# Performance work log

Hardware: AMD Instinct MI355X
Metric: run time of the kernel (lower is better)

The kernel has to match this reference:

```python
import jax, jax.numpy as jnp
import numpy as np

H, W = 512, 512
N = H * W
NCLS = 4
D_BI, D_SP = 5, 2
THETA_ALPHA, THETA_BETA, THETA_GAMMA = 80.0, 0.0625, 3.0
BI_COMPAT, SP_COMPAT, COMPATIBILITY = 10.0, 3.0, -1.0
NUM_ITER = 10


def _build_lattice(feats):
    """Permutohedral lattice precompute (numpy, integer index construction).
    feats: [N, d]. Returns os [N,d+1] int32 (1-based), ws [N,d+1] float32,
    bn [d+1, M, 2] int32 (0 = missing neighbor), M."""
    feats = np.asarray(feats, np.float64)
    n, d = feats.shape
    inv_std = np.sqrt(2.0 / 3.0) * (d + 1)
    scale = inv_std / np.sqrt((np.arange(d) + 1.0) * (np.arange(d) + 2.0))
    cf = feats * scale
    # embedding matrix E: elevated = cf @ E.T lies on the hyperplane sum=0
    E = np.zeros((d + 1, d))
    E[0, :] = 1.0
    for j in range(1, d + 1):
        E[j, j:] = 1.0
        E[j, j - 1] = -j
    elevated = cf @ E.T  # [n, d+1]
    greedy = (np.rint(elevated / (d + 1)) * (d + 1)).astype(np.int64)
    diff = elevated - greedy
    idx = np.arange(d + 1)
    upper = idx[None, :] > idx[:, None]
    lower = idx[None, :] < idx[:, None]
    di = diff[:, :, None]
    dj = diff[:, None, :]
    rank = (((dj > di) & upper) | ((dj >= di) & lower)).sum(-1)
    rank = rank + greedy.sum(1, keepdims=True) // (d + 1)
    low = rank < 0
    rank = rank + np.where(low, d + 1, 0)
    greedy = greedy + np.where(low, d + 1, 0)
    high = rank > d
    rank = rank - np.where(high, d + 1, 0)
    greedy = greedy - np.where(high, d + 1, 0)
    # barycentric weights
    bary = np.zeros((n, d + 2))
    v = (elevated - greedy) / (d + 1)
    rows = np.repeat(np.arange(n), d + 1)
    np.add.at(bary, (rows, (d - rank).ravel()), v.ravel())
    np.add.at(bary, (rows, (d + 1 - rank).ravel()), -v.ravel())
    bary[:, 0] += 1.0 + bary[:, d + 1]
    ws = bary[:, : d + 1].astype(np.float32)
    # simplex vertex keys (first d coords; last is implied by zero-sum)
    keys = np.empty((n, d + 1, d), np.int64)
    for r in range(d + 1):
        keys[:, r, :] = (greedy + r - (d + 1) * (rank > d - r))[:, :d]
    flat = keys.reshape(-1, d)
    lo = flat.min(0) - (d + 1)
    hi = flat.max(0) + (d + 1)
    strides = np.cumprod(np.concatenate([[1], (hi - lo + 1)[:-1]]))
    coords = (flat - lo) @ strides
    uniq, first, inv = np.unique(coords, return_index=True, return_inverse=True)
    M = int(len(uniq))
    os_ = (inv.reshape(n, d + 1) + 1).astype(np.int32)
    ukeys = flat[first]
    bn = np.zeros((d + 1, M, 2), np.int32)
    for j in range(d + 1):
        n1 = ukeys - 1
        n2 = ukeys + 1
        if j < d:
            n1[:, j] = ukeys[:, j] + d
            n2[:, j] = ukeys[:, j] - d
        for t, nk in enumerate((n1, n2)):
            c = (nk - lo) @ strides
            pos = np.clip(np.searchsorted(uniq, c), 0, M - 1)
            bn[j, :, t] = np.where(uniq[pos] == c, pos + 1, 0)
    return os_, ws, bn, M


def setup_inputs() -> dict:
    key = jax.random.key(0)
    k1, k2 = jax.random.split(key)
    image = jax.random.uniform(k1, (H, W, 7), dtype=jnp.float32)
    unary = jax.random.normal(k2, (H, W, NCLS), dtype=jnp.float32)
    img = np.asarray(image)
    yy, xx = np.mgrid[0:H, 0:W].astype(np.float64)
    bifeat = np.concatenate(
        [(xx / THETA_ALPHA)[..., None], (yy / THETA_ALPHA)[..., None],
         img[..., :3] / THETA_BETA], axis=-1).reshape(N, D_BI)
    spfeat = np.stack([xx / THETA_GAMMA, yy / THETA_GAMMA], -1).reshape(N, D_SP)
    os_b, ws_b, bn_b, M_b = _build_lattice(bifeat)
    os_s, ws_s, bn_s, M_s = _build_lattice(spfeat)
    return {
        "unary": unary,
        "ws_bilateral": jnp.asarray(ws_b), "os_bilateral": jnp.asarray(os_b),
        "blur_neighbors_bilateral": jnp.asarray(bn_b), "M_bilateral": M_b,
        "ws_spatial": jnp.asarray(ws_s), "os_spatial": jnp.asarray(os_s),
        "blur_neighbors_spatial": jnp.asarray(bn_s), "M_spatial": M_s,
    }


def _perm_filter(values, os_, ws, bn, M, alpha):
    # values: [N, C]; splat -> blur -> slice
    d1 = os_.shape[1]
    C = values.shape[1]
    table = jnp.zeros((M + 1, C), values.dtype)  # row 0 = dummy (missing)
    table = table.at[os_.reshape(-1)].add(
        (values[:, None, :] * ws[:, :, None]).reshape(-1, C))
    for j in range(d1):  # [0.5, 1, 0.5] blur along each lattice axis
        table = table.at[1:].add(0.5 * (table[bn[j, :, 0]] + table[bn[j, :, 1]]))
    return alpha * jnp.einsum("nrc,nr->nc", table[os_], ws)


def _mean_field(unary, ws_b, os_b, bn_b, M_b, ws_s, os_s, bn_s, M_s):
    C = unary.shape[-1]
    u = unary.reshape(N, C)
    alpha_b = 1.0 / (1.0 + 2.0 ** (-D_BI))
    alpha_s = 1.0 / (1.0 + 2.0 ** (-D_SP))
    ones = jnp.ones((N, 1), u.dtype)
    inv_nb = 1.0 / (_perm_filter(ones, os_b, ws_b, bn_b, M_b, alpha_b) + 1e-20)
    inv_ns = 1.0 / (_perm_filter(ones, os_s, ws_s, bn_s, M_s, alpha_s) + 1e-20)
    Q = jax.nn.softmax(-u, axis=-1)
    for _ in range(NUM_ITER):
        msg = (BI_COMPAT * _perm_filter(Q, os_b, ws_b, bn_b, M_b, alpha_b) * inv_nb
               + SP_COMPAT * _perm_filter(Q, os_s, ws_s, bn_s, M_s, alpha_s) * inv_ns)
        Q = jax.nn.softmax(-u - COMPATIBILITY * msg, axis=-1)
    return Q.reshape(H, W, C)


def reference(unary, ws_bilateral, os_bilateral, blur_neighbors_bilateral, M_bilateral,
              ws_spatial, os_spatial, blur_neighbors_spatial, M_spatial):
    # Returns the refined marginals Q [H, W, NCLS]; the module's MAP output is
    # jnp.argmax(Q, -1) (kept soft here so fwd/bwd share one output).
    return _mean_field(unary, ws_bilateral, os_bilateral, blur_neighbors_bilateral,
                       M_bilateral, ws_spatial, os_spatial, blur_neighbors_spatial,
                       M_spatial)
```

## Files before the change

kernel.cpp:

```cpp
#include <hip/hip_runtime.h>

#define NPIX (512 * 512)
#define BLK 256

#define SCAN_T 256
#define SCAN_E 8
#define SCAN_CHUNK (SCAN_T * SCAN_E)

constexpr float ALPHA_B = 32.0f / 33.0f;
constexpr float ALPHA_S = 0.8f;
constexpr float BI_COMPAT = 10.0f;
constexpr float SP_COMPAT = 3.0f;

__device__ __forceinline__ unsigned pack_ent(int n, float w) {
    float wc = fminf(fmaxf(w, 0.f), 1.f);
    unsigned iw = (unsigned)(wc * 16383.f + 0.5f);
    return (iw << 18) | (unsigned)n;
}
__device__ __forceinline__ int ent_pix(unsigned e) { return (int)(e & 0x3FFFFu); }
__device__ __forceinline__ float ent_w(unsigned e) {
    return (float)(e >> 18) * (1.0f / 16383.0f);
}

__device__ __forceinline__ float4 f4zero() { return make_float4(0.f, 0.f, 0.f, 0.f); }

__device__ __forceinline__ float4 f4_eval1(const float4* __restrict__ t,
                                           const int* __restrict__ bn, int x) {
    int b1 = bn[2 * (x - 1)], b2 = bn[2 * (x - 1) + 1];
    float4 a = t[x], u = t[b1], v = t[b2];
    return make_float4(a.x + 0.5f * (u.x + v.x),
                       a.y + 0.5f * (u.y + v.y),
                       a.z + 0.5f * (u.z + v.z),
                       a.w + 0.5f * (u.w + v.w));
}
__device__ __forceinline__ float4 f4_eval2(const float4* __restrict__ t,
                                           const int* __restrict__ bnA,
                                           const int* __restrict__ bnB, int x) {
    int a1 = bnB[2 * (x - 1)], a2 = bnB[2 * (x - 1) + 1];
    float4 r = f4_eval1(t, bnA, x);
    if (a1) {
        float4 q = f4_eval1(t, bnA, a1);
        r.x += 0.5f * q.x; r.y += 0.5f * q.y; r.z += 0.5f * q.z; r.w += 0.5f * q.w;
    }
    if (a2) {
        float4 q = f4_eval1(t, bnA, a2);
        r.x += 0.5f * q.x; r.y += 0.5f * q.y; r.z += 0.5f * q.z; r.w += 0.5f * q.w;
    }
    return r;
}

__device__ __forceinline__ float f_eval1(const float* __restrict__ t,
                                         const int* __restrict__ bn, int x) {
    int b1 = bn[2 * (x - 1)], b2 = bn[2 * (x - 1) + 1];
    return t[x] + 0.5f * (t[b1] + t[b2]);
}
__device__ __forceinline__ float f_eval2(const float* __restrict__ t,
                                         const int* __restrict__ bnA,
                                         const int* __restrict__ bnB, int x) {
    int a1 = bnB[2 * (x - 1)], a2 = bnB[2 * (x - 1) + 1];
    float r = f_eval1(t, bnA, x);
    if (a1) r += 0.5f * f_eval1(t, bnA, a1);
    if (a2) r += 0.5f * f_eval1(t, bnA, a2);
    return r;
}

__global__ void k_softmax_init(const float4* __restrict__ u, float4* __restrict__ Q) {
    int n = blockIdx.x * BLK + threadIdx.x;
    if (n >= NPIX) return;
    float4 uu = u[n];
    float l0 = -uu.x, l1 = -uu.y, l2 = -uu.z, l3 = -uu.w;
    float m = fmaxf(fmaxf(l0, l1), fmaxf(l2, l3));
    float e0 = expf(l0 - m), e1 = expf(l1 - m), e2 = expf(l2 - m), e3 = expf(l3 - m);
    float inv = 1.0f / (e0 + e1 + e2 + e3);
    Q[n] = make_float4(e0 * inv, e1 * inv, e2 * inv, e3 * inv);
}

__global__ void k_count_softmax(const int* __restrict__ osb, const int* __restrict__ oss,
                                int* __restrict__ cntB, int* __restrict__ cntS,
                                const float4* __restrict__ u, float4* __restrict__ Q) {
    int n = blockIdx.x * BLK + threadIdx.x;
    if (n >= NPIX) return;
    float4 uu = u[n];
    float l0 = -uu.x, l1 = -uu.y, l2 = -uu.z, l3 = -uu.w;
    float m = fmaxf(fmaxf(l0, l1), fmaxf(l2, l3));
    float e0 = expf(l0 - m), e1 = expf(l1 - m), e2 = expf(l2 - m), e3 = expf(l3 - m);
    float inv = 1.0f / (e0 + e1 + e2 + e3);
    Q[n] = make_float4(e0 * inv, e1 * inv, e2 * inv, e3 * inv);
#pragma unroll
    for (int r = 0; r < 6; r++) atomicAdd(&cntB[osb[n * 6 + r]], 1);
#pragma unroll
    for (int r = 0; r < 3; r++) atomicAdd(&cntS[oss[n * 3 + r]], 1);
}

__global__ void k_chunk_sum(const int* __restrict__ counts, int V, int* __restrict__ csum) {
    __shared__ int lds[SCAN_T];
    int base = blockIdx.x * SCAN_CHUNK;
    int s = 0;
#pragma unroll
    for (int j = 0; j < SCAN_E; j++) {
        int idx = base + threadIdx.x * SCAN_E + j;
        if (idx < V) s += counts[idx];
    }
    lds[threadIdx.x] = s;
    __syncthreads();
    for (int off = SCAN_T / 2; off > 0; off >>= 1) {
        if ((int)threadIdx.x < off) lds[threadIdx.x] += lds[threadIdx.x + off];
        __syncthreads();
    }
    if (threadIdx.x == 0) csum[blockIdx.x] = lds[0];
}

__global__ void k_scan_csum(int* __restrict__ csum, int nchunks) {
    __shared__ int lds[SCAN_T];
    int carry = 0;
    for (int base = 0; base < nchunks; base += SCAN_T) {
        int idx = base + threadIdx.x;
        int v = (idx < nchunks) ? csum[idx] : 0;
        lds[threadIdx.x] = v;
        __syncthreads();
        for (int off = 1; off < SCAN_T; off <<= 1) {
            int t = ((int)threadIdx.x >= off) ? lds[threadIdx.x - off] : 0;
            __syncthreads();
            lds[threadIdx.x] += t;
            __syncthreads();
        }
        int incl = lds[threadIdx.x];
        int tile_total = lds[SCAN_T - 1];
        if (idx < nchunks) csum[idx] = incl - v + carry;
        carry += tile_total;
        __syncthreads();
    }
}

__global__ void k_chunk_scan(const int* __restrict__ counts, int V,
                             const int* __restrict__ csum, int* __restrict__ start,
                             int* __restrict__ cursor) {
    __shared__ int lds[SCAN_T];
    int base = blockIdx.x * SCAN_CHUNK;
    int local[SCAN_E];
    int s = 0;
#pragma unroll
    for (int j = 0; j < SCAN_E; j++) {
        int idx = base + threadIdx.x * SCAN_E + j;
        int c = (idx < V) ? counts[idx] : 0;
        local[j] = c;
        s += c;
    }
    lds[threadIdx.x] = s;
    __syncthreads();
    for (int off = 1; off < SCAN_T; off <<= 1) {
        int t = ((int)threadIdx.x >= off) ? lds[threadIdx.x - off] : 0;
        __syncthreads();
        lds[threadIdx.x] += t;
        __syncthreads();
    }
    int excl = lds[threadIdx.x] - s + csum[blockIdx.x];
#pragma unroll
    for (int j = 0; j < SCAN_E; j++) {
        int idx = base + threadIdx.x * SCAN_E + j;
        if (idx < V) { start[idx] = excl; cursor[idx] = excl; }
        excl += local[j];
    }
}

__global__ void k_fill_both(const int* __restrict__ osb, const float* __restrict__ wsb,
                            int* __restrict__ curB, unsigned* __restrict__ entB,
                            const int* __restrict__ oss, const float* __restrict__ wss,
                            int* __restrict__ curS, unsigned* __restrict__ entS) {
    int n = blockIdx.x * BLK + threadIdx.x;
    if (n >= NPIX) return;
#pragma unroll
    for (int r = 0; r < 6; r++) {
        int o = osb[n * 6 + r];
        int pos = atomicAdd(&curB[o], 1);
        entB[pos] = pack_ent(n, wsb[n * 6 + r]);
    }
#pragma unroll
    for (int r = 0; r < 3; r++) {
        int o = oss[n * 3 + r];
        int pos = atomicAdd(&curS[o], 1);
        entS[pos] = pack_ent(n, wss[n * 3 + r]);
    }
}

__global__ void k_gather1_both(const unsigned* __restrict__ entB, const int* __restrict__ startB,
                               int totB, int Vb, float* __restrict__ nB,
                               const unsigned* __restrict__ entS, const int* __restrict__ startS,
                               int totS, int Vs, float* __restrict__ nS) {
    int i = blockIdx.x * BLK + threadIdx.x;
    const unsigned* ent; const int* st; int tot, V, idx; float* out;
    if (i < Vb) { ent = entB; st = startB; tot = totB; V = Vb; out = nB; idx = i; }
    else {
        idx = i - Vb;
        if (idx >= Vs) return;
        ent = entS; st = startS; tot = totS; V = Vs; out = nS;
    }
    int s = st[idx];
    int e = (idx + 1 < V) ? st[idx + 1] : tot;
    float acc = 0.f;
    for (int k = s; k < e; k++) acc += ent_w(ent[k]);
    out[idx] = acc;
}

__global__ void k_gather4f_both(const unsigned* __restrict__ entB, const int* __restrict__ startB,
                                int totB, int Vb, float4* __restrict__ tB,
                                const unsigned* __restrict__ entS, const int* __restrict__ startS,
                                int totS, int Vs, float4* __restrict__ tS,
                                const float4* __restrict__ Q) {
    int i = blockIdx.x * BLK + threadIdx.x;
    const unsigned* ent; const int* st; int tot, V, idx; float4* out;
    if (i < Vb) { ent = entB; st = startB; tot = totB; V = Vb; out = tB; idx = i; }
    else {
        idx = i - Vb;
        if (idx >= Vs) return;
        ent = entS; st = startS; tot = totS; V = Vs; out = tS;
    }
    int s = st[idx];
    int e = (idx + 1 < V) ? st[idx + 1] : tot;
    float4 acc = f4zero();
    for (int k = s; k < e; k++) {
        unsigned en = ent[k];
        float w = ent_w(en);
        float4 q = Q[ent_pix(en)];
        acc.x += w * q.x; acc.y += w * q.y; acc.z += w * q.z; acc.w += w * q.w;
    }
    out[idx] = acc;
}

__global__ void k_cblur4f_both(const float4* __restrict__ inB, float4* __restrict__ outB,
                               const int* __restrict__ bnb, int Mb,
                               const float4* __restrict__ inS, float4* __restrict__ outS,
                               const int* __restrict__ bns, int Ms) {
    int i = blockIdx.x * BLK + threadIdx.x;
    if (i <= Mb) {
        if (i == 0) { outB[0] = f4zero(); return; }
        outB[i] = f4_eval2(inB, bnb, bnb + (size_t)Mb * 2, i);
        return;
    }
    int idx = i - (Mb + 1);
    if (idx > Ms) return;
    if (idx == 0) { outS[0] = f4zero(); return; }
    const int* sn0 = bns;
    const int* sn1 = bns + (size_t)Ms * 2;
    const int* sn2 = bns + (size_t)Ms * 4;
    int c1 = sn2[2 * (idx - 1)], c2 = sn2[2 * (idx - 1) + 1];
    float4 r = f4_eval2(inS, sn0, sn1, idx);
    if (c1) {
        float4 q = f4_eval2(inS, sn0, sn1, c1);
        r.x += 0.5f * q.x; r.y += 0.5f * q.y; r.z += 0.5f * q.z; r.w += 0.5f * q.w;
    }
    if (c2) {
        float4 q = f4_eval2(inS, sn0, sn1, c2);
        r.x += 0.5f * q.x; r.y += 0.5f * q.y; r.z += 0.5f * q.z; r.w += 0.5f * q.w;
    }
    outS[idx] = r;
}

__global__ void k_cblur4f(const float4* __restrict__ in, float4* __restrict__ out,
                          const int* __restrict__ bnA, const int* __restrict__ bnB_, int M) {
    int i = blockIdx.x * BLK + threadIdx.x;
    if (i > M) return;
    if (i == 0) { out[0] = f4zero(); return; }
    out[i] = f4_eval2(in, bnA, bnB_, i);
}

__global__ void k_cblur1_both(const float* __restrict__ inB, float* __restrict__ outB,
                              const int* __restrict__ bnb, int Mb,
                              const float* __restrict__ inS, float* __restrict__ outS,
                              const int* __restrict__ bns, int Ms) {
    int i = blockIdx.x * BLK + threadIdx.x;
    if (i <= Mb) {
        if (i == 0) { outB[0] = 0.f; return; }
        outB[i] = f_eval2(inB, bnb, bnb + (size_t)Mb * 2, i);
        return;
    }
    int idx = i - (Mb + 1);
    if (idx > Ms) return;
    if (idx == 0) { outS[0] = 0.f; return; }
    const int* sn0 = bns;
    const int* sn1 = bns + (size_t)Ms * 2;
    const int* sn2 = bns + (size_t)Ms * 4;
    int c1 = sn2[2 * (idx - 1)], c2 = sn2[2 * (idx - 1) + 1];
    float r = f_eval2(inS, sn0, sn1, idx);
    if (c1) r += 0.5f * f_eval2(inS, sn0, sn1, c1);
    if (c2) r += 0.5f * f_eval2(inS, sn0, sn1, c2);
    outS[idx] = r;
}

__global__ void k_cblur1(const float* __restrict__ in, float* __restrict__ out,
                         const int* __restrict__ bnA, const int* __restrict__ bnB_, int M) {
    int i = blockIdx.x * BLK + threadIdx.x;
    if (i > M) return;
    if (i == 0) { out[0] = 0.f; return; }
    out[i] = f_eval2(in, bnA, bnB_, i);
}

__global__ void k_norm_prescale(const float* __restrict__ nTb, const float* __restrict__ wsb,
                                const int* __restrict__ osb,
                                const float* __restrict__ nTs, const float* __restrict__ wss,
                                const int* __restrict__ oss,
                                float* __restrict__ wsbp, float* __restrict__ wssp) {
    int n = blockIdx.x * BLK + threadIdx.x;
    if (n >= NPIX) return;
    float sb = 0.f;
#pragma unroll
    for (int r = 0; r < 6; r++) sb += wsb[n * 6 + r] * nTb[osb[n * 6 + r]];
    float cb = BI_COMPAT * ALPHA_B / (ALPHA_B * sb + 1e-20f);
#pragma unroll
    for (int r = 0; r < 6; r++) wsbp[n * 6 + r] = wsb[n * 6 + r] * cb;
    float ss = 0.f;
#pragma unroll
    for (int r = 0; r < 3; r++) ss += wss[n * 3 + r] * nTs[oss[n * 3 + r]];
    float cs = SP_COMPAT * ALPHA_S / (ALPHA_S * ss + 1e-20f);
#pragma unroll
    for (int r = 0; r < 3; r++) wssp[n * 3 + r] = wss[n * 3 + r] * cs;
}

__global__ void k_slice_combine_f(const float4* __restrict__ u,
                                  const float4* __restrict__ tb, const float* __restrict__ wsbp,
                                  const int* __restrict__ osb,
                                  const float4* __restrict__ ts, const float* __restrict__ wssp,
                                  const int* __restrict__ oss,
                                  float4* __restrict__ Qout) {
    int n = blockIdx.x * BLK + threadIdx.x;
    if (n >= NPIX) return;
    float4 uu = u[n];
    float l0 = -uu.x, l1 = -uu.y, l2 = -uu.z, l3 = -uu.w;
#pragma unroll
    for (int r = 0; r < 6; r++) {
        float w = wsbp[n * 6 + r];
        float4 t = tb[osb[n * 6 + r]];
        l0 += w * t.x; l1 += w * t.y; l2 += w * t.z; l3 += w * t.w;
    }
#pragma unroll
    for (int r = 0; r < 3; r++) {
        float w = wssp[n * 3 + r];
        float4 t = ts[oss[n * 3 + r]];
        l0 += w * t.x; l1 += w * t.y; l2 += w * t.z; l3 += w * t.w;
    }
    float m = fmaxf(fmaxf(l0, l1), fmaxf(l2, l3));
    float e0 = expf(l0 - m), e1 = expf(l1 - m), e2 = expf(l2 - m), e3 = expf(l3 - m);
    float inv = 1.0f / (e0 + e1 + e2 + e3);
    Qout[n] = make_float4(e0 * inv, e1 * inv, e2 * inv, e3 * inv);
}

template <int D1>
__global__ void k_splat1(const float* __restrict__ ws, const int* __restrict__ os,
                         float* __restrict__ table) {
    int n = blockIdx.x * BLK + threadIdx.x;
    if (n >= NPIX) return;
#pragma unroll
    for (int r = 0; r < D1; r++) atomicAdd(&table[os[n * D1 + r]], ws[n * D1 + r]);
}

template <int D1>
__global__ void k_splat4(const float4* __restrict__ Q, const float* __restrict__ ws,
                         const int* __restrict__ os, float* __restrict__ table) {
    int n = blockIdx.x * BLK + threadIdx.x;
    if (n >= NPIX) return;
    float4 q = Q[n];
#pragma unroll
    for (int r = 0; r < D1; r++) {
        float w = ws[n * D1 + r];
        int o = os[n * D1 + r];
        float* t = table + 4 * (size_t)o;
        atomicAdd(t + 0, q.x * w);
        atomicAdd(t + 1, q.y * w);
        atomicAdd(t + 2, q.z * w);
        atomicAdd(t + 3, q.w * w);
    }
}

__global__ void k_blur1(const float* __restrict__ in, float* __restrict__ out,
                        const int* __restrict__ bn, int M) {
    int i = blockIdx.x * BLK + threadIdx.x;
    if (i > M) return;
    if (i == 0) { out[0] = 0.f; return; }
    int n1 = bn[(size_t)(i - 1) * 2 + 0];
    int n2 = bn[(size_t)(i - 1) * 2 + 1];
    out[i] = in[i] + 0.5f * (in[n1] + in[n2]);
}

__global__ void k_blur4(const float4* __restrict__ in, float4* __restrict__ out,
                        const int* __restrict__ bn, int M) {
    int i = blockIdx.x * BLK + threadIdx.x;
    if (i > M) return;
    if (i == 0) { out[0] = f4zero(); return; }
    int n1 = bn[(size_t)(i - 1) * 2 + 0];
    int n2 = bn[(size_t)(i - 1) * 2 + 1];
    float4 a = in[i], b = in[n1], c = in[n2];
    out[i] = make_float4(a.x + 0.5f * (b.x + c.x), a.y + 0.5f * (b.y + c.y),
                         a.z + 0.5f * (b.z + c.z), a.w + 0.5f * (b.w + c.w));
}

template <int D1>
__global__ void k_norm_slice(const float* __restrict__ table, const float* __restrict__ ws,
                             const int* __restrict__ os, float alpha,
                             float* __restrict__ inv_out) {
    int n = blockIdx.x * BLK + threadIdx.x;
    if (n >= NPIX) return;
    float s = 0.f;
#pragma unroll
    for (int r = 0; r < D1; r++) s += ws[n * D1 + r] * table[os[n * D1 + r]];
    inv_out[n] = 1.0f / (alpha * s + 1e-20f);
}

__global__ void k_slice_combine(const float4* __restrict__ u,
                                const float4* __restrict__ tb, const float* __restrict__ wsb,
                                const int* __restrict__ osb,
                                const float4* __restrict__ ts, const float* __restrict__ wss,
                                const int* __restrict__ oss,
                                const float* __restrict__ inv_nb,
                                const float* __restrict__ inv_ns,
                                float4* __restrict__ Qout) {
    int n = blockIdx.x * BLK + threadIdx.x;
    if (n >= NPIX) return;
    float4 ab = f4zero();
#pragma unroll
    for (int r = 0; r < 6; r++) {
        float w = wsb[n * 6 + r];
        float4 t = tb[osb[n * 6 + r]];
        ab.x += w * t.x; ab.y += w * t.y; ab.z += w * t.z; ab.w += w * t.w;
    }
    float4 as = f4zero();
#pragma unroll
    for (int r = 0; r < 3; r++) {
        float w = wss[n * 3 + r];
        float4 t = ts[oss[n * 3 + r]];
        as.x += w * t.x; as.y += w * t.y; as.z += w * t.z; as.w += w * t.w;
    }
    float cb = BI_COMPAT * ALPHA_B * inv_nb[n];
    float cs = SP_COMPAT * ALPHA_S * inv_ns[n];
    float4 uu = u[n];
    float l0 = -uu.x + cb * ab.x + cs * as.x;
    float l1 = -uu.y + cb * ab.y + cs * as.y;
    float l2 = -uu.z + cb * ab.z + cs * as.z;
    float l3 = -uu.w + cb * ab.w + cs * as.w;
    float m = fmaxf(fmaxf(l0, l1), fmaxf(l2, l3));
    float e0 = expf(l0 - m), e1 = expf(l1 - m), e2 = expf(l2 - m), e3 = expf(l3 - m);
    float inv = 1.0f / (e0 + e1 + e2 + e3);
    Qout[n] = make_float4(e0 * inv, e1 * inv, e2 * inv, e3 * inv);
}

extern "C" void kernel_launch(void* const* d_in, const int* in_sizes, int n_in,
                              void* d_out, int out_size, void* d_ws, size_t ws_size,
                              hipStream_t stream) {
    const float* unary = (const float*)d_in[0];
    const float* wsb   = (const float*)d_in[1];
    const int*   osb   = (const int*)d_in[2];
    const int*   bnb   = (const int*)d_in[3];
    const float* wss   = (const float*)d_in[5];
    const int*   oss   = (const int*)d_in[6];
    const int*   bns   = (const int*)d_in[7];
    const int Mb = in_sizes[3] / 12;
    const int Ms = in_sizes[7] / 6;
    const int Vb = Mb + 1, Vs = Ms + 1;
    const int totB = NPIX * 6, totS = NPIX * 3;

    float* Q = (float*)d_out;

    char* p = (char*)d_ws;
    auto alloc = [&](size_t nbytes) -> void* {
        void* r = (void*)p;
        p += (nbytes + 15) & ~(size_t)15;
        return r;
    };
    float4* tAb = (float4*)alloc((size_t)Vb * 16);
    float4* tBb = (float4*)alloc((size_t)Vb * 16);
    float4* tAs = (float4*)alloc((size_t)Vs * 16);
    float4* tBs = (float4*)alloc((size_t)Vs * 16);
    float* nAb = (float*)alloc((size_t)Vb * 4);
    float* nBb = (float*)alloc((size_t)Vb * 4);
    float* nAs = (float*)alloc((size_t)Vs * 4);
    float* nBs = (float*)alloc((size_t)Vs * 4);
    float* wsbp = (float*)alloc((size_t)NPIX * 6 * 4);
    float* wssp = (float*)alloc((size_t)NPIX * 3 * 4);
    int*  startB  = (int*)alloc((size_t)Vb * 4);
    int*  cursorB = (int*)alloc((size_t)Vb * 4);
    unsigned* entB = (unsigned*)alloc((size_t)totB * 4);
    int*  startS  = (int*)alloc((size_t)Vs * 4);
    int*  cursorS = (int*)alloc((size_t)Vs * 4);
    unsigned* entS = (unsigned*)alloc((size_t)totS * 4);
    int*  csum    = (int*)alloc(8192 * 4);
    size_t need = (size_t)(p - (char*)d_ws);
    bool use_gather = need <= ws_size;

    dim3 blk(BLK);
    dim3 gN((NPIX + BLK - 1) / BLK);
    dim3 gVb((Vb + BLK - 1) / BLK);
    dim3 gVBS((Vb + Vs + BLK - 1) / BLK);

    const int* bnb2 = bnb + (size_t)2 * Mb * 2;
    const int* bnb3 = bnb + (size_t)3 * Mb * 2;
    const int* bnb4 = bnb + (size_t)4 * Mb * 2;
    const int* bnb5 = bnb + (size_t)5 * Mb * 2;

    if (use_gather) {
        int nchB = (Vb + SCAN_CHUNK - 1) / SCAN_CHUNK;
        int nchS = (Vs + SCAN_CHUNK - 1) / SCAN_CHUNK;
        hipMemsetAsync(cursorB, 0, (size_t)Vb * 4, stream);
        hipMemsetAsync(cursorS, 0, (size_t)Vs * 4, stream);
        k_count_softmax<<<gN, blk, 0, stream>>>(osb, oss, cursorB, cursorS,
                                                (const float4*)unary, (float4*)Q);
        k_chunk_sum<<<dim3(nchB), dim3(SCAN_T), 0, stream>>>(cursorB, Vb, csum);
        k_scan_csum<<<dim3(1), dim3(SCAN_T), 0, stream>>>(csum, nchB);
        k_chunk_scan<<<dim3(nchB), dim3(SCAN_T), 0, stream>>>(cursorB, Vb, csum, startB, cursorB);
        k_chunk_sum<<<dim3(nchS), dim3(SCAN_T), 0, stream>>>(cursorS, Vs, csum);
        k_scan_csum<<<dim3(1), dim3(SCAN_T), 0, stream>>>(csum, nchS);
        k_chunk_scan<<<dim3(nchS), dim3(SCAN_T), 0, stream>>>(cursorS, Vs, csum, startS, cursorS);
        k_fill_both<<<gN, blk, 0, stream>>>(osb, wsb, cursorB, entB, oss, wss, cursorS, entS);

        k_gather1_both<<<gVBS, blk, 0, stream>>>(entB, startB, totB, Vb, nAb,
                                                 entS, startS, totS, Vs, nAs);
        k_cblur1_both<<<gVBS, blk, 0, stream>>>(nAb, nBb, bnb, Mb, nAs, nBs, bns, Ms);
        k_cblur1<<<gVb, blk, 0, stream>>>(nBb, nAb, bnb2, bnb3, Mb);
        k_cblur1<<<gVb, blk, 0, stream>>>(nAb, nBb, bnb4, bnb5, Mb);
        k_norm_prescale<<<gN, blk, 0, stream>>>(nBb, wsb, osb, nBs, wss, oss, wsbp, wssp);

        for (int it = 0; it < 10; it++) {
            k_gather4f_both<<<gVBS, blk, 0, stream>>>(entB, startB, totB, Vb, tAb,
                                                      entS, startS, totS, Vs, tAs,
                                                      (const float4*)Q);
            k_cblur4f_both<<<gVBS, blk, 0, stream>>>(tAb, tBb, bnb, Mb, tAs, tBs, bns, Ms);
            k_cblur4f<<<gVb, blk, 0, stream>>>(tBb, tAb, bnb2, bnb3, Mb);
            k_cblur4f<<<gVb, blk, 0, stream>>>(tAb, tBb, bnb4, bnb5, Mb);
            k_slice_combine_f<<<gN, blk, 0, stream>>>((const float4*)unary,
                                                      tBb, wsbp, osb, tBs, wssp, oss,
                                                      (float4*)Q);
        }
    } else {
        char* q = (char*)d_ws;
        auto alloc2 = [&](size_t nbytes) -> void* {
            void* r = (void*)q;
            q += (nbytes + 15) & ~(size_t)15;
            return r;
        };
        float* fAb = (float*)alloc2((size_t)Vb * 4 * sizeof(float));
        float* fBb = (float*)alloc2((size_t)Vb * 4 * sizeof(float));
        float* fAs = (float*)alloc2((size_t)Vs * 4 * sizeof(float));
        float* fBs = (float*)alloc2((size_t)Vs * 4 * sizeof(float));
        float* inv_nb = (float*)alloc2(NPIX * sizeof(float));
        float* inv_ns = (float*)alloc2(NPIX * sizeof(float));
        dim3 gMb((Mb + 1 + BLK - 1) / BLK);
        dim3 gMs((Ms + 1 + BLK - 1) / BLK);

        hipMemsetAsync(fAb, 0, (size_t)Vb * sizeof(float), stream);
        k_splat1<6><<<gN, blk, 0, stream>>>(wsb, osb, fAb);
        {
            float* a = fAb; float* b = fBb;
            for (int j = 0; j < 6; j++) {
                k_blur1<<<gMb, blk, 0, stream>>>(a, b, bnb + (size_t)j * Mb * 2, Mb);
                float* t = a; a = b; b = t;
            }
            k_norm_slice<6><<<gN, blk, 0, stream>>>(a, wsb, osb, ALPHA_B, inv_nb);
        }
        hipMemsetAsync(fAs, 0, (size_t)Vs * sizeof(float), stream);
        k_splat1<3><<<gN, blk, 0, stream>>>(wss, oss, fAs);
        {
            float* a = fAs; float* b = fBs;
            for (int j = 0; j < 3; j++) {
                k_blur1<<<gMs, blk, 0, stream>>>(a, b, bns + (size_t)j * Ms * 2, Ms);
                float* t = a; a = b; b = t;
            }
            k_norm_slice<3><<<gN, blk, 0, stream>>>(a, wss, oss, ALPHA_S, inv_ns);
        }
        k_softmax_init<<<gN, blk, 0, stream>>>((const float4*)unary, (float4*)Q);
        for (int it = 0; it < 10; it++) {
            hipMemsetAsync(fAb, 0, (size_t)Vb * 4 * sizeof(float), stream);
            k_splat4<6><<<gN, blk, 0, stream>>>((const float4*)Q, wsb, osb, fAb);
            float* a = fAb; float* b = fBb;
            for (int j = 0; j < 6; j++) {
                k_blur4<<<gMb, blk, 0, stream>>>((const float4*)a, (float4*)b,
                                                 bnb + (size_t)j * Mb * 2, Mb);
                float* t = a; a = b; b = t;
            }
            float* finb = a;
            hipMemsetAsync(fAs, 0, (size_t)Vs * 4 * sizeof(float), stream);
            k_splat4<3><<<gN, blk, 0, stream>>>((const float4*)Q, wss, oss, fAs);
            float* as_ = fAs; float* bs_ = fBs;
            for (int j = 0; j < 3; j++) {
                k_blur4<<<gMs, blk, 0, stream>>>((const float4*)as_, (float4*)bs_,
                                                 bns + (size_t)j * Ms * 2, Ms);
                float* t = as_; as_ = bs_; bs_ = t;
            }
            float* fins = as_;
            k_slice_combine<<<gN, blk, 0, stream>>>((const float4*)unary,
                                                    (const float4*)finb, wsb, osb,
                                                    (const float4*)fins, wss, oss,
                                                    inv_nb, inv_ns, (float4*)Q);
        }
    }
}
```

Before: 1.019 ms.

## Replace bilateral CSR scatter build with atomicExch linked lists

For the bilateral lattice, the count/scan/fill CSR construction is replaced by per-vertex linked lists built with atomicExch, which removes the count pass and three scan kernels for that lattice. The gather kernels now follow linked-list pointers, and each entry grows to an int2. This saves setup work, but each of the 10 iterations now does dependent, scattered pointer-chasing loads in place of contiguous CSR reads, which probably costs more than the setup it saves. The spatial lattice keeps its CSR path, and the blur helpers are refactored into eval3 functions.

```diff
diff --git a/kernel.cpp b/kernel.cpp
--- a/kernel.cpp
+++ b/kernel.cpp
@@ -28,10 +28,8 @@
                                            const int* __restrict__ bn, int x) {
     int b1 = bn[2 * (x - 1)], b2 = bn[2 * (x - 1) + 1];
     float4 a = t[x], u = t[b1], v = t[b2];
-    return make_float4(a.x + 0.5f * (u.x + v.x),
-                       a.y + 0.5f * (u.y + v.y),
-                       a.z + 0.5f * (u.z + v.z),
-                       a.w + 0.5f * (u.w + v.w));
+    return make_float4(a.x + 0.5f * (u.x + v.x), a.y + 0.5f * (u.y + v.y),
+                       a.z + 0.5f * (u.z + v.z), a.w + 0.5f * (u.w + v.w));
 }
 __device__ __forceinline__ float4 f4_eval2(const float4* __restrict__ t,
                                            const int* __restrict__ bnA,
@@ -48,6 +46,22 @@
     }
     return r;
 }
+__device__ __forceinline__ float4 f4_eval3(const float4* __restrict__ t,
+                                           const int* __restrict__ bn0,
+                                           const int* __restrict__ bn1,
+                                           const int* __restrict__ bn2, int x) {
+    int c1 = bn2[2 * (x - 1)], c2 = bn2[2 * (x - 1) + 1];
+    float4 r = f4_eval2(t, bn0, bn1, x);
+    if (c1) {
+        float4 q = f4_eval2(t, bn0, bn1, c1);
+        r.x += 0.5f * q.x; r.y += 0.5f * q.y; r.z += 0.5f * q.z; r.w += 0.5f * q.w;
+    }
+    if (c2) {
+        float4 q = f4_eval2(t, bn0, bn1, c2);
+        r.x += 0.5f * q.x; r.y += 0.5f * q.y; r.z += 0.5f * q.z; r.w += 0.5f * q.w;
+    }
+    return r;
+}
 
 __device__ __forceinline__ float f_eval1(const float* __restrict__ t,
                                          const int* __restrict__ bn, int x) {
@@ -63,8 +77,19 @@
     if (a2) r += 0.5f * f_eval1(t, bnA, a2);
     return r;
 }
-
-__global__ void k_softmax_init(const float4* __restrict__ u, float4* __restrict__ Q) {
+__device__ __forceinline__ float f_eval3(const float* __restrict__ t,
+                                         const int* __restrict__ bn0,
+                                         const int* __restrict__ bn1,
+                                         const int* __restrict__ bn2, int x) {
+    int c1 = bn2[2 * (x - 1)], c2 = bn2[2 * (x - 1) + 1];
+    float r = f_eval2(t, bn0, bn1, x);
+    if (c1) r += 0.5f * f_eval2(t, bn0, bn1, c1);
+    if (c2) r += 0.5f * f_eval2(t, bn0, bn1, c2);
+    return r;
+}
+
+__global__ void k_softmax_count(const float4* __restrict__ u, float4* __restrict__ Q,
+                                const int* __restrict__ oss, int* __restrict__ cntS) {
     int n = blockIdx.x * BLK + threadIdx.x;
     if (n >= NPIX) return;
     float4 uu = u[n];
@@ -73,21 +98,6 @@
     float e0 = expf(l0 - m), e1 = expf(l1 - m), e2 = expf(l2 - m), e3 = expf(l3 - m);
     float inv = 1.0f / (e0 + e1 + e2 + e3);
     Q[n] = make_float4(e0 * inv, e1 * inv, e2 * inv, e3 * inv);
-}
-
-__global__ void k_count_softmax(const int* __restrict__ osb, const int* __restrict__ oss,
-                                int* __restrict__ cntB, int* __restrict__ cntS,
-                                const float4* __restrict__ u, float4* __restrict__ Q) {
-    int n = blockIdx.x * BLK + threadIdx.x;
-    if (n >= NPIX) return;
-    float4 uu = u[n];
-    float l0 = -uu.x, l1 = -uu.y, l2 = -uu.z, l3 = -uu.w;
-    float m = fmaxf(fmaxf(l0, l1), fmaxf(l2, l3));
-    float e0 = expf(l0 - m), e1 = expf(l1 - m), e2 = expf(l2 - m), e3 = expf(l3 - m);
-    float inv = 1.0f / (e0 + e1 + e2 + e3);
-    Q[n] = make_float4(e0 * inv, e1 * inv, e2 * inv, e3 * inv);
-#pragma unroll
-    for (int r = 0; r < 6; r++) atomicAdd(&cntB[osb[n * 6 + r]], 1);
 #pragma unroll
     for (int r = 0; r < 3; r++) atomicAdd(&cntS[oss[n * 3 + r]], 1);
 }
@@ -98,7 +108,7 @@
     int s = 0;
 #pragma unroll
     for (int j = 0; j < SCAN_E; j++) {
-        int idx = base + threadIdx.x * SCAN_E + j;
+        int idx = base + (int)threadIdx.x * SCAN_E + j;
         if (idx < V) s += counts[idx];
     }
     lds[threadIdx.x] = s;
@@ -114,7 +124,7 @@
     __shared__ int lds[SCAN_T];
     int carry = 0;
     for (int base = 0; base < nchunks; base += SCAN_T) {
-        int idx = base + threadIdx.x;
+        int idx = base + (int)threadIdx.x;
         int v = (idx < nchunks) ? csum[idx] : 0;
         lds[threadIdx.x] = v;
         __syncthreads();
@@ -141,7 +151,7 @@
     int s = 0;
 #pragma unroll
     for (int j = 0; j < SCAN_E; j++) {
-        int idx = base + threadIdx.x * SCAN_E + j;
+        int idx = base + (int)threadIdx.x * SCAN_E + j;
         int c = (idx < V) ? counts[idx] : 0;
         local[j] = c;
         s += c;
@@ -157,23 +167,24 @@
     int excl = lds[threadIdx.x] - s + csum[blockIdx.x];
 #pragma unroll
     for (int j = 0; j < SCAN_E; j++) {
-        int idx = base + threadIdx.x * SCAN_E + j;
+        int idx = base + (int)threadIdx.x * SCAN_E + j;
         if (idx < V) { start[idx] = excl; cursor[idx] = excl; }
         excl += local[j];
     }
 }
 
-__global__ void k_fill_both(const int* __restrict__ osb, const float* __restrict__ wsb,
-                            int* __restrict__ curB, unsigned* __restrict__ entB,
-                            const int* __restrict__ oss, const float* __restrict__ wss,
-                            int* __restrict__ curS, unsigned* __restrict__ entS) {
+__global__ void k_fill2(const int* __restrict__ osb, const float* __restrict__ wsb,
+                        int* __restrict__ headB, int2* __restrict__ entB2,
+                        const int* __restrict__ oss, const float* __restrict__ wss,
+                        int* __restrict__ curS, unsigned* __restrict__ entS) {
     int n = blockIdx.x * BLK + threadIdx.x;
     if (n >= NPIX) return;
 #pragma unroll
     for (int r = 0; r < 6; r++) {
         int o = osb[n * 6 + r];
-        int pos = atomicAdd(&curB[o], 1);
-        entB[pos] = pack_ent(n, wsb[n * 6 + r]);
+        int idx = n * 6 + r;
+        int old = atomicExch(&headB[o], idx);
+        entB2[idx] = make_int2((int)pack_ent(n, wsb[n * 6 + r]), old);
     }
 #pragma unroll
     for (int r = 0; r < 3; r++) {
@@ -183,48 +194,62 @@
     }
 }
 
-__global__ void k_gather1_both(const unsigned* __restrict__ entB, const int* __restrict__ startB,
-                               int totB, int Vb, float* __restrict__ nB,
+__global__ void k_gather1_both(const int* __restrict__ headB, const int2* __restrict__ entB2,
+                               int Vb, float* __restrict__ nB,
                                const unsigned* __restrict__ entS, const int* __restrict__ startS,
                                int totS, int Vs, float* __restrict__ nS) {
     int i = blockIdx.x * BLK + threadIdx.x;
-    const unsigned* ent; const int* st; int tot, V, idx; float* out;
-    if (i < Vb) { ent = entB; st = startB; tot = totB; V = Vb; out = nB; idx = i; }
-    else {
-        idx = i - Vb;
-        if (idx >= Vs) return;
-        ent = entS; st = startS; tot = totS; V = Vs; out = nS;
-    }
-    int s = st[idx];
-    int e = (idx + 1 < V) ? st[idx + 1] : tot;
+    if (i < Vb) {
+        int j = headB[i];
+        float acc = 0.f;
+        while (j >= 0) {
+            int2 e = entB2[j];
+            acc += ent_w((unsigned)e.x);
+            j = e.y;
+        }
+        nB[i] = acc;
+        return;
+    }
+    int idx = i - Vb;
+    if (idx >= Vs) return;
+    int s = startS[idx];
+    int e = (idx + 1 < Vs) ? startS[idx + 1] : totS;
     float acc = 0.f;
-    for (int k = s; k < e; k++) acc += ent_w(ent[k]);
-    out[idx] = acc;
-}
-
-__global__ void k_gather4f_both(const unsigned* __restrict__ entB, const int* __restrict__ startB,
-                                int totB, int Vb, float4* __restrict__ tB,
+    for (int k = s; k < e; k++) acc += ent_w(entS[k]);
+    nS[idx] = acc;
+}
+
+__global__ void k_gather4f_both(const int* __restrict__ headB, const int2* __restrict__ entB2,
+                                int Vb, float4* __restrict__ tB,
                                 const unsigned* __restrict__ entS, const int* __restrict__ startS,
                                 int totS, int Vs, float4* __restrict__ tS,
                                 const float4* __restrict__ Q) {
     int i = blockIdx.x * BLK + threadIdx.x;
-    const unsigned* ent; const int* st; int tot, V, idx; float4* out;
-    if (i < Vb) { ent = entB; st = startB; tot = totB; V = Vb; out = tB; idx = i; }
-    else {
-        idx = i - Vb;
-        if (idx >= Vs) return;
-        ent = entS; st = startS; tot = totS; V = Vs; out = tS;
-    }
-    int s = st[idx];
-    int e = (idx + 1 < V) ? st[idx + 1] : tot;
+    if (i < Vb) {
+        int j = headB[i];
+        float4 acc = f4zero();
+        while (j >= 0) {
+            int2 e = entB2[j];
+            float w = ent_w((unsigned)e.x);
+            float4 q = Q[ent_pix((unsigned)e.x)];
+            acc.x += w * q.x; acc.y += w * q.y; acc.z += w * q.z; acc.w += w * q.w;
+            j = e.y;
+        }
+        tB[i] = acc;
+        return;
+    }
+    int idx = i - Vb;
+    if (idx >= Vs) return;
+    int s = startS[idx];
+    int e = (idx + 1 < Vs) ? startS[idx + 1] : totS;
     float4 acc = f4zero();
     for (int k = s; k < e; k++) {
-        unsigned en = ent[k];
+        unsigned en = entS[k];
         float w = ent_w(en);
         float4 q = Q[ent_pix(en)];
         acc.x += w * q.x; acc.y += w * q.y; acc.z += w * q.z; acc.w += w * q.w;
     }
-    out[idx] = acc;
+    tS[idx] = acc;
 }
 
 __global__ void k_cblur4f_both(const float4* __restrict__ inB, float4* __restrict__ outB,
@@ -240,20 +265,7 @@
     int idx = i - (Mb + 1);
     if (idx > Ms) return;
     if (idx == 0) { outS[0] = f4zero(); return; }
-    const int* sn0 = bns;
-    const int* sn1 = bns + (size_t)Ms * 2;
-    const int* sn2 = bns + (size_t)Ms * 4;
-    int c1 = sn2[2 * (idx - 1)], c2 = sn2[2 * (idx - 1) + 1];
-    float4 r = f4_eval2(inS, sn0, sn1, idx);
-    if (c1) {
-        float4 q = f4_eval2(inS, sn0, sn1, c1);
-        r.x += 0.5f * q.x; r.y += 0.5f * q.y; r.z += 0.5f * q.z; r.w += 0.5f * q.w;
-    }
-    if (c2) {
-        float4 q = f4_eval2(inS, sn0, sn1, c2);
-        r.x += 0.5f * q.x; r.y += 0.5f * q.y; r.z += 0.5f * q.z; r.w += 0.5f * q.w;
-    }
-    outS[idx] = r;
+    outS[idx] = f4_eval3(inS, bns, bns + (size_t)Ms * 2, bns + (size_t)Ms * 4, idx);
 }
 
 __global__ void k_cblur4f(const float4* __restrict__ in, float4* __restrict__ out,
@@ -277,14 +289,7 @@
     int idx = i - (Mb + 1);
     if (idx > Ms) return;
     if (idx == 0) { outS[0] = 0.f; return; }
-    const int* sn0 = bns;
-    const int* sn1 = bns + (size_t)Ms * 2;
-    const int* sn2 = bns + (size_t)Ms * 4;
-    int c1 = sn2[2 * (idx - 1)], c2 = sn2[2 * (idx - 1) + 1];
-    float r = f_eval2(inS, sn0, sn1, idx);
-    if (c1) r += 0.5f * f_eval2(inS, sn0, sn1, c1);
-    if (c2) r += 0.5f * f_eval2(inS, sn0, sn1, c2);
-    outS[idx] = r;
+    outS[idx] = f_eval3(inS, bns, bns + (size_t)Ms * 2, bns + (size_t)Ms * 4, idx);
 }
 
 __global__ void k_cblur1(const float* __restrict__ in, float* __restrict__ out,
@@ -342,6 +347,17 @@
     float e0 = expf(l0 - m), e1 = expf(l1 - m), e2 = expf(l2 - m), e3 = expf(l3 - m);
     float inv = 1.0f / (e0 + e1 + e2 + e3);
     Qout[n] = make_float4(e0 * inv, e1 * inv, e2 * inv, e3 * inv);
+}
+
+__global__ void k_softmax_init(const float4* __restrict__ u, float4* __restrict__ Q) {
+    int n = blockIdx.x * BLK + threadIdx.x;
+    if (n >= NPIX) return;
+    float4 uu = u[n];
+    float l0 = -uu.x, l1 = -uu.y, l2 = -uu.z, l3 = -uu.w;
+    float m = fmaxf(fmaxf(l0, l1), fmaxf(l2, l3));
+    float e0 = expf(l0 - m), e1 = expf(l1 - m), e2 = expf(l2 - m), e3 = expf(l3 - m);
+    float inv = 1.0f / (e0 + e1 + e2 + e3);
+    Q[n] = make_float4(e0 * inv, e1 * inv, e2 * inv, e3 * inv);
 }
 
 template <int D1>
@@ -475,13 +491,12 @@
     float* nBs = (float*)alloc((size_t)Vs * 4);
     float* wsbp = (float*)alloc((size_t)NPIX * 6 * 4);
     float* wssp = (float*)alloc((size_t)NPIX * 3 * 4);
-    int*  startB  = (int*)alloc((size_t)Vb * 4);
-    int*  cursorB = (int*)alloc((size_t)Vb * 4);
-    unsigned* entB = (unsigned*)alloc((size_t)totB * 4);
+    int*  headB  = (int*)alloc((size_t)Vb * 4);
+    int2* entB2  = (int2*)alloc((size_t)totB * 8);
     int*  startS  = (int*)alloc((size_t)Vs * 4);
     int*  cursorS = (int*)alloc((size_t)Vs * 4);
     unsigned* entS = (unsigned*)alloc((size_t)totS * 4);
-    int*  csum    = (int*)alloc(8192 * 4);
+    int*  csumS   = (int*)alloc(8192 * 4);
     size_t need = (size_t)(p - (char*)d_ws);
     bool use_gather = need <= ws_size;
 
@@ -496,21 +511,19 @@
     const int* bnb5 = bnb + (size_t)5 * Mb * 2;
 
     if (use_gather) {
-        int nchB = (Vb + SCAN_CHUNK - 1) / SCAN_CHUNK;
         int nchS = (Vs + SCAN_CHUNK - 1) / SCAN_CHUNK;
-        hipMemsetAsync(cursorB, 0, (size_t)Vb * 4, stream);
+        hipMemsetAsync(headB, 0xFF, (size_t)Vb * 4, stream);
         hipMemsetAsync(cursorS, 0, (size_t)Vs * 4, stream);
-        k_count_softmax<<<gN, blk, 0, stream>>>(osb, oss, cursorB, cursorS,
-                                                (const float4*)unary, (float4*)Q);
-        k_chunk_sum<<<dim3(nchB), dim3(SCAN_T), 0, stream>>>(cursorB, Vb, csum);
-        k_scan_csum<<<dim3(1), dim3(SCAN_T), 0, stream>>>(csum, nchB);
-        k_chunk_scan<<<dim3(nchB), dim3(SCAN_T), 0, stream>>>(cursorB, Vb, csum, startB, cursorB);
-        k_chunk_sum<<<dim3(nchS), dim3(SCAN_T), 0, stream>>>(cursorS, Vs, csum);
-        k_scan_csum<<<dim3(1), dim3(SCAN_T), 0, stream>>>(csum, nchS);
-        k_chunk_scan<<<dim3(nchS), dim3(SCAN_T), 0, stream>>>(cursorS, Vs, csum, startS, cursorS);
-        k_fill_both<<<gN, blk, 0, stream>>>(osb, wsb, cursorB, entB, oss, wss, cursorS, entS);
-
-        k_gather1_both<<<gVBS, blk, 0, stream>>>(entB, startB, totB, Vb, nAb,
+        k_softmax_count<<<gN, blk, 0, stream>>>((const float4*)unary, (float4*)Q,
+                                                oss, cursorS);
+        k_chunk_sum<<<dim3(nchS), dim3(SCAN_T), 0, stream>>>(cursorS, Vs, csumS);
+        k_scan_csum<<<dim3(1), dim3(SCAN_T), 0, stream>>>(csumS, nchS);
+        k_chunk_scan<<<dim3(nchS), dim3(SCAN_T), 0, stream>>>(cursorS, Vs, csumS,
+                                                              startS, cursorS);
+        k_fill2<<<gN, blk, 0, stream>>>(osb, wsb, headB, entB2,
+                                        oss, wss, cursorS, entS);
+
+        k_gather1_both<<<gVBS, blk, 0, stream>>>(headB, entB2, Vb, nAb,
                                                  entS, startS, totS, Vs, nAs);
         k_cblur1_both<<<gVBS, blk, 0, stream>>>(nAb, nBb, bnb, Mb, nAs, nBs, bns, Ms);
         k_cblur1<<<gVb, blk, 0, stream>>>(nBb, nAb, bnb2, bnb3, Mb);
@@ -518,7 +531,7 @@
         k_norm_prescale<<<gN, blk, 0, stream>>>(nBb, wsb, osb, nBs, wss, oss, wsbp, wssp);
 
         for (int it = 0; it < 10; it++) {
-            k_gather4f_both<<<gVBS, blk, 0, stream>>>(entB, startB, totB, Vb, tAb,
+            k_gather4f_both<<<gVBS, blk, 0, stream>>>(headB, entB2, Vb, tAb,
                                                       entS, startS, totS, Vs, tAs,
                                                       (const float4*)Q);
             k_cblur4f_both<<<gVBS, blk, 0, stream>>>(tAb, tBb, bnb, Mb, tAs, tBs, bns, Ms);
```

After: 1.201 ms. +17.9%, slower.
